# Kernel optimization log

Measured on AMD Instinct MI355X. Metric: run time of the kernel, lower is better.

The kernel has to match this reference:

```python
import jax, jax.numpy as jnp
import numpy as np

EMBED_DIM = 1024
BATCH = 4
SEQ = 4096


def setup_inputs() -> dict:
    key = jax.random.key(0)
    k1, k2, k3, k4 = jax.random.split(key, 4)
    return {
        "inputs": jax.random.normal(k1, (BATCH, SEQ, EMBED_DIM), dtype=jnp.float32),
        "Wq": jax.random.normal(k2, (EMBED_DIM, EMBED_DIM), dtype=jnp.float32),
        "Wk": jax.random.normal(k3, (EMBED_DIM, EMBED_DIM), dtype=jnp.float32),
        "Wv": jax.random.normal(k4, (EMBED_DIM, EMBED_DIM), dtype=jnp.float32),
    }


def reference(inputs, Wq, Wk, Wv):
    # inputs: [B, N, D]
    d = inputs.shape[-1]
    q = inputs @ Wq  # [B, N, D]
    k = inputs @ Wk
    v = inputs @ Wv
    scale = 1.0 / jnp.sqrt(jnp.asarray(d, dtype=inputs.dtype))
    logits = jnp.einsum("bnd,bmd->bnm", q, k) * scale  # [B, N, N]
    scores = jax.nn.softmax(logits, axis=-1)
    out = jnp.einsum("bnm,bmd->bnd", scores, v)  # [B, N, D]
    return out.mean(axis=-1)  # [B, N]
```

## Files before the change

### kernel.cpp

```cpp
#include <hip/hip_runtime.h>

#define EMBED 1024
#define BATCH 4
#define SEQ   4096
#define ROWS  (BATCH*SEQ)
#define CAP   128
#define TSCAN_SC 140.0f
#define TRES  160.0f

typedef __attribute__((ext_vector_type(8))) short bf16x8;
typedef __attribute__((ext_vector_type(4))) float f32x4;
typedef __attribute__((ext_vector_type(4))) int   i32x4;

static __device__ __forceinline__ unsigned short f2bf(float x) {
    unsigned u = __float_as_uint(x);
    u = (u + 0x7fffu + ((u >> 16) & 1u)) >> 16;
    return (unsigned short)u;
}
static __device__ __forceinline__ float bf2f(unsigned short h) {
    return __uint_as_float(((unsigned)h) << 16);
}
static __device__ __forceinline__ void split2(float x, unsigned short& hi, unsigned short& lo) {
    hi = f2bf(x);
    lo = f2bf(x - bf2f(hi));
}

static __device__ __forceinline__ void gll(const unsigned short* g, unsigned short* l) {
    __builtin_amdgcn_global_load_lds(
        (const __attribute__((address_space(1))) unsigned int*)g,
        (__attribute__((address_space(3))) unsigned int*)l, 16, 0, 0);
}
static __device__ __forceinline__ void gllb(const unsigned char* g, unsigned char* l) {
    __builtin_amdgcn_global_load_lds(
        (const __attribute__((address_space(1))) unsigned int*)g,
        (__attribute__((address_space(3))) unsigned int*)l, 16, 0, 0);
}
static __device__ __forceinline__ void stage_tile(unsigned short (*lds)[32],
                                                  const unsigned short* gbase,
                                                  int wave, int lane) {
#pragma unroll
    for (int c = 0; c < 2; c++) {
        int L = wave * 128 + c * 64 + lane;
        int r = L >> 2, s = L & 3;
        int g = (s - (r >> 1)) & 3;
        gll(gbase + (size_t)r * EMBED + g * 8, &lds[r][s * 8]);
    }
}
static __device__ __forceinline__ bf16x8 read_frag(const unsigned short (*lds)[32], int r, int kq) {
    int s = ((kq >> 3) + (r >> 1)) & 3;
    return *(const bf16x8*)&lds[r][s * 8];
}
static __device__ __forceinline__ void stage_tile8(unsigned char (*lds)[64],
                                                   const unsigned char* gbase,
                                                   int wave, int lane) {
#pragma unroll
    for (int c = 0; c < 2; c++) {
        int L = wave * 128 + c * 64 + lane;
        int r = L >> 2, s = L & 3;
        int g = (s - (r >> 1)) & 3;
        gllb(gbase + (size_t)r * EMBED + g * 16, &lds[r][s * 16]);
    }
}
static __device__ __forceinline__ i32x4 read_frag8(const unsigned char (*lds)[64], int r, int kseg) {
    int s = (kseg + (r >> 1)) & 3;
    return *(const i32x4*)&lds[r][s * 16];
}

__global__ void k_wvbar(const float* __restrict__ Wv, float* __restrict__ wvbar) {
    int r = blockIdx.x, t = threadIdx.x;
    float s = 0.f;
    for (int c = t; c < EMBED; c += 256) s += Wv[(size_t)r * EMBED + c];
    for (int d = 1; d < 64; d <<= 1) s += __shfl_xor(s, d);
    __shared__ float ws_[4];
    if ((t & 63) == 0) ws_[t >> 6] = s;
    __syncthreads();
    if (t == 0) wvbar[r] = (ws_[0] + ws_[1] + ws_[2] + ws_[3]) * (1.0f / EMBED);
}

__global__ __launch_bounds__(256) void k_xsplit_vmean(
    const float* __restrict__ X, const float* __restrict__ wvbar,
    unsigned short* __restrict__ Xhi, unsigned short* __restrict__ Xlo,
    float* __restrict__ vmean, int* __restrict__ cnt,
    signed char* __restrict__ X8, float* __restrict__ scaleX) {
    int row = blockIdx.x, t = threadIdx.x;
    float4 x4 = *(const float4*)(X + (size_t)row * EMBED + t * 4);
    float4 w4 = *(const float4*)(wvbar + t * 4);
    ushort4 h, l;
    split2(x4.x, h.x, l.x); split2(x4.y, h.y, l.y);
    split2(x4.z, h.z, l.z); split2(x4.w, h.w, l.w);
    *(ushort4*)(Xhi + (size_t)row * EMBED + t * 4) = h;
    *(ushort4*)(Xlo + (size_t)row * EMBED + t * 4) = l;
    float s = x4.x * w4.x + x4.y * w4.y + x4.z * w4.z + x4.w * w4.w;
    float am = fmaxf(fmaxf(fabsf(x4.x), fabsf(x4.y)), fmaxf(fabsf(x4.z), fabsf(x4.w)));
    for (int d = 1; d < 64; d <<= 1) {
        s += __shfl_xor(s, d);
        am = fmaxf(am, __shfl_xor(am, d));
    }
    __shared__ float ws_[4], wa_[4];
    if ((t & 63) == 0) { ws_[t >> 6] = s; wa_[t >> 6] = am; }
    __syncthreads();
    if (t == 0) { vmean[row] = ws_[0] + ws_[1] + ws_[2] + ws_[3]; cnt[row] = 0; }
    if (X8) {
        float bm = fmaxf(fmaxf(wa_[0], wa_[1]), fmaxf(wa_[2], wa_[3]));
        bm = fmaxf(bm, 1e-20f);
        float inv = 127.0f / bm;
        char4 q;
        q.x = (signed char)(int)rintf(x4.x * inv);
        q.y = (signed char)(int)rintf(x4.y * inv);
        q.z = (signed char)(int)rintf(x4.z * inv);
        q.w = (signed char)(int)rintf(x4.w * inv);
        *(char4*)(X8 + (size_t)row * EMBED + t * 4) = q;
        if (t == 0) scaleX[row] = bm * (1.0f / 127.0f);
    }
}

__global__ __launch_bounds__(256) void k_tquant(
    const unsigned short* __restrict__ Thi,
    signed char* __restrict__ T8, float* __restrict__ scaleT) {
    int row = blockIdx.x, t = threadIdx.x;
    ushort4 h = *(const ushort4*)(Thi + (size_t)row * EMBED + t * 4);
    float f0 = bf2f(h.x), f1 = bf2f(h.y), f2 = bf2f(h.z), f3 = bf2f(h.w);
    float am = fmaxf(fmaxf(fabsf(f0), fabsf(f1)), fmaxf(fabsf(f2), fabsf(f3)));
    for (int d = 1; d < 64; d <<= 1) am = fmaxf(am, __shfl_xor(am, d));
    __shared__ float wa_[4];
    if ((t & 63) == 0) wa_[t >> 6] = am;
    __syncthreads();
    float bm = fmaxf(fmaxf(fmaxf(wa_[0], wa_[1]), fmaxf(wa_[2], wa_[3])), 1e-20f);
    float inv = 127.0f / bm;
    char4 q;
    q.x = (signed char)(int)rintf(f0 * inv);
    q.y = (signed char)(int)rintf(f1 * inv);
    q.z = (signed char)(int)rintf(f2 * inv);
    q.w = (signed char)(int)rintf(f3 * inv);
    *(char4*)(T8 + (size_t)row * EMBED + t * 4) = q;
    if (t == 0) scaleT[row] = bm * (1.0f / 127.0f);
}

__global__ __launch_bounds__(256) void k_gemm3(
    const unsigned short* __restrict__ Ahi, const unsigned short* __restrict__ Alo,
    const unsigned short* __restrict__ BThi, const unsigned short* __restrict__ BTlo,
    unsigned short* __restrict__ Chi, unsigned short* __restrict__ Clo) {
    __shared__ unsigned short Ah[128][32], Al[128][32], Bh[128][32], Bl[128][32];
    int bx = blockIdx.x;
    int bm = bx >> 3, bn = bx & 7;
    int tid = threadIdx.x, wave = tid >> 6, lane = tid & 63;
    int wm = (wave >> 1) * 64, wn = (wave & 1) * 64;
    int mrow = lane & 15, kq = (lane >> 4) * 8;

    f32x4 zero = {0.f, 0.f, 0.f, 0.f};
    f32x4 acc[4][4];
    for (int a = 0; a < 4; a++) for (int b = 0; b < 4; b++) acc[a][b] = zero;

    const unsigned short* Abase_h = Ahi + (size_t)(bm * 128) * EMBED;
    const unsigned short* Abase_l = Alo + (size_t)(bm * 128) * EMBED;
    const unsigned short* Bbase_h = BThi + (size_t)(bn * 128) * EMBED;
    const unsigned short* Bbase_l = BTlo + (size_t)(bn * 128) * EMBED;

    for (int k0 = 0; k0 < EMBED; k0 += 32) {
        __syncthreads();
        stage_tile(Ah, Abase_h + k0, wave, lane);
        stage_tile(Al, Abase_l + k0, wave, lane);
        stage_tile(Bh, Bbase_h + k0, wave, lane);
        stage_tile(Bl, Bbase_l + k0, wave, lane);
        __syncthreads();
        bf16x8 ah[4], al[4], bh[4], bl[4];
#pragma unroll
        for (int t = 0; t < 4; t++) {
            ah[t] = read_frag(Ah, wm + t * 16 + mrow, kq);
            al[t] = read_frag(Al, wm + t * 16 + mrow, kq);
            bh[t] = read_frag(Bh, wn + t * 16 + mrow, kq);
            bl[t] = read_frag(Bl, wn + t * 16 + mrow, kq);
        }
#pragma unroll
        for (int mt = 0; mt < 4; mt++)
#pragma unroll
            for (int nt = 0; nt < 4; nt++) {
                acc[mt][nt] = __builtin_amdgcn_mfma_f32_16x16x32_bf16(ah[mt], bh[nt], acc[mt][nt], 0, 0, 0);
                acc[mt][nt] = __builtin_amdgcn_mfma_f32_16x16x32_bf16(ah[mt], bl[nt], acc[mt][nt], 0, 0, 0);
                acc[mt][nt] = __builtin_amdgcn_mfma_f32_16x16x32_bf16(al[mt], bh[nt], acc[mt][nt], 0, 0, 0);
            }
    }
#pragma unroll
    for (int mt = 0; mt < 4; mt++)
#pragma unroll
        for (int nt = 0; nt < 4; nt++)
#pragma unroll
            for (int i = 0; i < 4; i++) {
                int row = bm * 128 + wm + mt * 16 + (lane >> 4) * 4 + i;
                int col = bn * 128 + wn + nt * 16 + (lane & 15);
                unsigned short h, l; split2(acc[mt][nt][i], h, l);
                Chi[(size_t)row * EMBED + col] = h;
                Clo[(size_t)row * EMBED + col] = l;
            }
}

__global__ __launch_bounds__(256, 3) void k_scan(
    const signed char* __restrict__ T8, const signed char* __restrict__ X8,
    const float* __restrict__ scaleT, const float* __restrict__ scaleX,
    int* __restrict__ cnt, int2* __restrict__ cand) {
    __shared__ unsigned char ThA[128][64], KhA[128][64];
    __shared__ unsigned char ThB[128][64], KhB[128][64];
    __shared__ float rowmax_[2][2][64];
    __shared__ float sT_[128], sX_[128];
    int bid = blockIdx.x;
    int x   = bid & 7;
    int i   = bid >> 3;
    int kbi = i & 3;
    int qb  = (i >> 2) & 31;
    int b   = i >> 7;
    int kb  = x * 4 + kbi;
    int tid = threadIdx.x, wave = tid >> 6, lane = tid & 63;
    int wr = wave >> 1, wc = wave & 1;
    int wq = wr * 64, wk = wc * 64;
    int mrow = lane & 15, kseg = lane >> 4;
    size_t qrow0 = (size_t)b * SEQ + (size_t)qb * 128;
    size_t krow0 = (size_t)b * SEQ + (size_t)kb * 128;
    const unsigned char* Tk = (const unsigned char*)T8 + qrow0 * EMBED;
    const unsigned char* Xk = (const unsigned char*)X8 + krow0 * EMBED;

    if (tid < 128) sT_[tid] = scaleT[qrow0 + tid];
    else           sX_[tid - 128] = scaleX[krow0 + tid - 128];

    i32x4 zero = {0, 0, 0, 0};
    i32x4 acc[4][4];
    for (int a = 0; a < 4; a++) for (int c = 0; c < 4; c++) acc[a][c] = zero;

    for (int k0 = 0; k0 < EMBED; k0 += 128) {
        __syncthreads();
        stage_tile8(ThA, Tk + k0,      wave, lane);
        stage_tile8(KhA, Xk + k0,      wave, lane);
        stage_tile8(ThB, Tk + k0 + 64, wave, lane);
        stage_tile8(KhB, Xk + k0 + 64, wave, lane);
        __syncthreads();
        {
            i32x4 ah[4], bh[4];
#pragma unroll
            for (int t = 0; t < 4; t++) {
                ah[t] = read_frag8(ThA, wq + t * 16 + mrow, kseg);
                bh[t] = read_frag8(KhA, wk + t * 16 + mrow, kseg);
            }
#pragma unroll
            for (int mt = 0; mt < 4; mt++)
#pragma unroll
                for (int nt = 0; nt < 4; nt++)
                    acc[mt][nt] = __builtin_amdgcn_mfma_i32_16x16x64_i8(ah[mt], bh[nt], acc[mt][nt], 0, 0, 0);
        }
        {
            i32x4 ah[4], bh[4];
#pragma unroll
            for (int t = 0; t < 4; t++) {
                ah[t] = read_frag8(ThB, wq + t * 16 + mrow, kseg);
                bh[t] = read_frag8(KhB, wk + t * 16 + mrow, kseg);
            }
#pragma unroll
            for (int mt = 0; mt < 4; mt++)
#pragma unroll
                for (int nt = 0; nt < 4; nt++)
                    acc[mt][nt] = __builtin_amdgcn_mfma_i32_16x16x64_i8(ah[mt], bh[nt], acc[mt][nt], 0, 0, 0);
        }
    }

#pragma unroll
    for (int mt = 0; mt < 4; mt++)
#pragma unroll
        for (int i2 = 0; i2 < 4; i2++) {
            int lr = mt * 16 + (lane >> 4) * 4 + i2;
            float st = sT_[wq + lr] * 0.03125f;
            float v = -INFINITY;
#pragma unroll
            for (int nt = 0; nt < 4; nt++) {
                float sc = (float)acc[mt][nt][i2] * sX_[wk + nt * 16 + (lane & 15)];
                v = fmaxf(v, sc);
            }
            v *= st;
#pragma unroll
            for (int d = 1; d < 16; d <<= 1) v = fmaxf(v, __shfl_xor(v, d));
            if ((lane & 15) == 0) rowmax_[wc][wr][lr] = v;
        }
    __syncthreads();
#pragma unroll
    for (int mt = 0; mt < 4; mt++)
#pragma unroll
        for (int i2 = 0; i2 < 4; i2++) {
            int lr = mt * 16 + (lane >> 4) * 4 + i2;
            float st = sT_[wq + lr] * 0.03125f;
            float th = fmaxf(rowmax_[0][wr][lr], rowmax_[1][wr][lr]) - TSCAN_SC;
            int grow = (int)qrow0 + wq + lr;
            int lpos = lane & 15;
            unsigned mm[4];
            float sc[4];
#pragma unroll
            for (int nt = 0; nt < 4; nt++) {
                sc[nt] = (float)acc[mt][nt][i2] * sX_[wk + nt * 16 + lpos] * st;
                unsigned long long bal = __ballot(sc[nt] >= th);
                mm[nt] = (unsigned)((bal >> (lane & 48)) & 0xFFFFull);
            }
            int tot = __popc(mm[0]) + __popc(mm[1]) + __popc(mm[2]) + __popc(mm[3]);
            if (tot > 0) {
                int base = 0;
                if (lpos == 0) base = atomicAdd(&cnt[grow], tot);
                base = __shfl(base, lane & 48);
                int run = base;
                unsigned below = (1u << lpos) - 1u;
#pragma unroll
                for (int nt = 0; nt < 4; nt++) {
                    if (mm[nt] & (1u << lpos)) {
                        int slot = run + __popc(mm[nt] & below);
                        if (slot < CAP) {
                            int gcol = (int)krow0 + wk + nt * 16 + lpos;
                            cand[(size_t)grow * CAP + slot] =
                                make_int2(gcol, __float_as_int(sc[nt]));
                        }
                    }
                    run += __popc(mm[nt]);
                }
            }
        }
}

__global__ __launch_bounds__(256) void k_rescore(
    const unsigned short* __restrict__ Thi, const unsigned short* __restrict__ Tlo,
    const float* __restrict__ X, const float* __restrict__ vmean,
    const int* __restrict__ cnt, const int2* __restrict__ cand,
    float* __restrict__ out) {
    int wave = threadIdx.x >> 6, lane = threadIdx.x & 63;
    int row = blockIdx.x * 4 + wave;
    int c = cnt[row]; if (c > CAP) c = CAP;
    const int2* cl = cand + (size_t)row * CAP;

    float smax = -INFINITY;
    for (int j = lane; j < c; j += 64) smax = fmaxf(smax, __int_as_float(cl[j].y));
    for (int d = 1; d < 64; d <<= 1) smax = fmaxf(smax, __shfl_xor(smax, d));
    float th = smax - TRES;

    float q[16];
    {
        const unsigned short* qh = Thi + (size_t)row * EMBED + lane * 16;
        const unsigned short* ql = Tlo + (size_t)row * EMBED + lane * 16;
        bf16x8 h0 = *(const bf16x8*)qh, h1 = *(const bf16x8*)(qh + 8);
        bf16x8 l0 = *(const bf16x8*)ql, l1 = *(const bf16x8*)(ql + 8);
#pragma unroll
        for (int i = 0; i < 8; i++) {
            q[i]     = bf2f((unsigned short)h0[i]) + bf2f((unsigned short)l0[i]);
            q[i + 8] = bf2f((unsigned short)h1[i]) + bf2f((unsigned short)l1[i]);
        }
    }

    __shared__ int   sm_[4][CAP];
    __shared__ float sl_[4][CAP];
    __shared__ int   ns_[4];
    if (lane == 0) ns_[wave] = 0;
    for (int j = lane; j < c; j += 64) {
        int2 p = cl[j];
        if (__int_as_float(p.y) >= th) {
            int idx = atomicAdd(&ns_[wave], 1);
            sm_[wave][idx] = p.x;
        }
    }
    int ns = ns_[wave];
    for (int t = 0; t < ns; t++) {
        int m = sm_[wave][t];
        const float* xr = X + (size_t)m * EMBED + lane * 16;
        float4 a0 = *(const float4*)(xr);
        float4 a1 = *(const float4*)(xr + 4);
        float4 a2 = *(const float4*)(xr + 8);
        float4 a3 = *(const float4*)(xr + 12);
        float dp = q[0]*a0.x + q[1]*a0.y + q[2]*a0.z + q[3]*a0.w
                 + q[4]*a1.x + q[5]*a1.y + q[6]*a1.z + q[7]*a1.w
                 + q[8]*a2.x + q[9]*a2.y + q[10]*a2.z + q[11]*a2.w
                 + q[12]*a3.x + q[13]*a3.y + q[14]*a3.z + q[15]*a3.w;
        for (int d = 1; d < 64; d <<= 1) dp += __shfl_xor(dp, d);
        if (lane == 0) sl_[wave][t] = dp * 0.03125f;
    }
    if (lane == 0) {
        float lm = -INFINITY;
        for (int t = 0; t < ns; t++) lm = fmaxf(lm, sl_[wave][t]);
        float den = 0.f, num = 0.f;
        for (int t = 0; t < ns; t++) {
            float e = __expf(sl_[wave][t] - lm);
            den += e;
            num += e * vmean[sm_[wave][t]];
        }
        out[row] = num / den;
    }
}

extern "C" void kernel_launch(void* const* d_in, const int* in_sizes, int n_in,
                              void* d_out, int out_size, void* d_ws, size_t ws_size,
                              hipStream_t stream) {
    const float* X  = (const float*)d_in[0];
    const float* Wq = (const float*)d_in[1];
    const float* Wk = (const float*)d_in[2];
    const float* Wv = (const float*)d_in[3];
    float* out = (float*)d_out;

    char* p = (char*)d_ws;
    auto alloc = [&](size_t bytes) -> void* {
        void* q = (void*)p;
        p += (bytes + 255) & ~(size_t)255;
        return q;
    };
    unsigned short* Wqhi = (unsigned short*)alloc((size_t)EMBED * EMBED * 2);
    unsigned short* Wqlo = (unsigned short*)alloc((size_t)EMBED * EMBED * 2);
    unsigned short* Wkhi = (unsigned short*)alloc((size_t)EMBED * EMBED * 2);
    unsigned short* Wklo = (unsigned short*)alloc((size_t)EMBED * EMBED * 2);
    unsigned short* MThi = (unsigned short*)alloc((size_t)EMBED * EMBED * 2);
    unsigned short* MTlo = (unsigned short*)alloc((size_t)EMBED * EMBED * 2);
    unsigned short* Xhi  = (unsigned short*)alloc((size_t)ROWS * EMBED * 2);
    unsigned short* Xlo  = (unsigned short*)alloc((size_t)ROWS * EMBED * 2);
    unsigned short* Thi  = (unsigned short*)alloc((size_t)ROWS * EMBED * 2);
    unsigned short* Tlo  = (unsigned short*)alloc((size_t)ROWS * EMBED * 2);
    signed char*    T8   = (signed char*)alloc((size_t)ROWS * EMBED);
    signed char*    X8   = (signed char*)alloc((size_t)ROWS * EMBED);
    float* scaleT = (float*)alloc((size_t)ROWS * 4);
    float* scaleX = (float*)alloc((size_t)ROWS * 4);
    float* wvbar = (float*)alloc(EMBED * 4);
    float* vmean = (float*)alloc((size_t)ROWS * 4);
    int*   cnt   = (int*)alloc((size_t)ROWS * 4);
    int2*  cand  = (int2*)alloc((size_t)ROWS * CAP * 8);

    k_wvbar<<<EMBED, 256, 0, stream>>>(Wv, wvbar);
    k_xsplit_vmean<<<EMBED, 256, 0, stream>>>(Wq, wvbar, Wqhi, Wqlo, vmean, cnt, nullptr, nullptr);
    k_xsplit_vmean<<<EMBED, 256, 0, stream>>>(Wk, wvbar, Wkhi, Wklo, vmean, cnt, nullptr, nullptr);
    k_gemm3<<<64, 256, 0, stream>>>(Wkhi, Wklo, Wqhi, Wqlo, MThi, MTlo);
    k_xsplit_vmean<<<ROWS, 256, 0, stream>>>(X, wvbar, Xhi, Xlo, vmean, cnt, X8, scaleX);
    k_gemm3<<<1024, 256, 0, stream>>>(Xhi, Xlo, MThi, MTlo, Thi, Tlo);
    k_tquant<<<ROWS, 256, 0, stream>>>(Thi, T8, scaleT);
    k_scan<<<4096, 256, 0, stream>>>(T8, X8, scaleT, scaleX, cnt, cand);
    k_rescore<<<ROWS / 4, 256, 0, stream>>>(Thi, Tlo, X, vmean, cnt, cand, out);
}
```

Baseline: 464.0 us.

## Replace atomic per-row candidate list with fixed per-tile slot buckets

The scan kernel no longer does a global atomicAdd per row to append candidates into a shared list. Each (row, key-block half) gets its own fixed region of SLOT entries plus a count, written without atomics. The epilogue is also restructured: the scale is applied once into the accumulators, and the threshold is divided by the row scale so the per-element multiply is skipped in the compare. The rescore kernel then reads all 512 slots per row, which raises its read traffic. Candidates beyond 8 per region are dropped, so accuracy depends on that cap.

```diff
diff --git a/kernel.cpp b/kernel.cpp
--- a/kernel.cpp
+++ b/kernel.cpp
@@ -4,9 +4,11 @@
 #define BATCH 4
 #define SEQ   4096
 #define ROWS  (BATCH*SEQ)
-#define CAP   128
 #define TSCAN_SC 140.0f
 #define TRES  160.0f
+#define KB2   64
+#define SLOT  8
+#define RESCAP 192
 
 typedef __attribute__((ext_vector_type(8))) short bf16x8;
 typedef __attribute__((ext_vector_type(4))) float f32x4;
@@ -80,7 +82,7 @@
 __global__ __launch_bounds__(256) void k_xsplit_vmean(
     const float* __restrict__ X, const float* __restrict__ wvbar,
     unsigned short* __restrict__ Xhi, unsigned short* __restrict__ Xlo,
-    float* __restrict__ vmean, int* __restrict__ cnt,
+    float* __restrict__ vmean, int* __restrict__ cnt2,
     signed char* __restrict__ X8, float* __restrict__ scaleX) {
     int row = blockIdx.x, t = threadIdx.x;
     float4 x4 = *(const float4*)(X + (size_t)row * EMBED + t * 4);
@@ -99,7 +101,8 @@
     __shared__ float ws_[4], wa_[4];
     if ((t & 63) == 0) { ws_[t >> 6] = s; wa_[t >> 6] = am; }
     __syncthreads();
-    if (t == 0) { vmean[row] = ws_[0] + ws_[1] + ws_[2] + ws_[3]; cnt[row] = 0; }
+    if (t == 0) vmean[row] = ws_[0] + ws_[1] + ws_[2] + ws_[3];
+    if (t < KB2) cnt2[(size_t)row * KB2 + t] = 0;
     if (X8) {
         float bm = fmaxf(fmaxf(wa_[0], wa_[1]), fmaxf(wa_[2], wa_[3]));
         bm = fmaxf(bm, 1e-20f);
@@ -197,7 +200,7 @@
 __global__ __launch_bounds__(256, 3) void k_scan(
     const signed char* __restrict__ T8, const signed char* __restrict__ X8,
     const float* __restrict__ scaleT, const float* __restrict__ scaleX,
-    int* __restrict__ cnt, int2* __restrict__ cand) {
+    int* __restrict__ cnt2, int2* __restrict__ cand2) {
     __shared__ unsigned char ThA[128][64], KhA[128][64];
     __shared__ unsigned char ThB[128][64], KhB[128][64];
     __shared__ float rowmax_[2][2][64];
@@ -263,73 +266,73 @@
 #pragma unroll
     for (int mt = 0; mt < 4; mt++)
 #pragma unroll
+        for (int nt = 0; nt < 4; nt++) {
+            float sx = sX_[wk + nt * 16 + (lane & 15)];
+#pragma unroll
+            for (int i2 = 0; i2 < 4; i2++)
+                acc[mt][nt][i2] = __float_as_int((float)acc[mt][nt][i2] * sx);
+        }
+#pragma unroll
+    for (int mt = 0; mt < 4; mt++)
+#pragma unroll
+        for (int i2 = 0; i2 < 4; i2++) {
+            float v = -INFINITY;
+#pragma unroll
+            for (int nt = 0; nt < 4; nt++) v = fmaxf(v, __int_as_float(acc[mt][nt][i2]));
+#pragma unroll
+            for (int d = 1; d < 16; d <<= 1) v = fmaxf(v, __shfl_xor(v, d));
+            if ((lane & 15) == 0) rowmax_[wc][wr][mt * 16 + (lane >> 4) * 4 + i2] = v;
+        }
+    __syncthreads();
+#pragma unroll
+    for (int mt = 0; mt < 4; mt++)
+#pragma unroll
         for (int i2 = 0; i2 < 4; i2++) {
             int lr = mt * 16 + (lane >> 4) * 4 + i2;
             float st = sT_[wq + lr] * 0.03125f;
-            float v = -INFINITY;
-#pragma unroll
-            for (int nt = 0; nt < 4; nt++) {
-                float sc = (float)acc[mt][nt][i2] * sX_[wk + nt * 16 + (lane & 15)];
-                v = fmaxf(v, sc);
-            }
-            v *= st;
-#pragma unroll
-            for (int d = 1; d < 16; d <<= 1) v = fmaxf(v, __shfl_xor(v, d));
-            if ((lane & 15) == 0) rowmax_[wc][wr][lr] = v;
-        }
-    __syncthreads();
-#pragma unroll
-    for (int mt = 0; mt < 4; mt++)
-#pragma unroll
-        for (int i2 = 0; i2 < 4; i2++) {
-            int lr = mt * 16 + (lane >> 4) * 4 + i2;
-            float st = sT_[wq + lr] * 0.03125f;
-            float th = fmaxf(rowmax_[0][wr][lr], rowmax_[1][wr][lr]) - TSCAN_SC;
+            float thr = fmaxf(rowmax_[0][wr][lr], rowmax_[1][wr][lr]) - TSCAN_SC / st;
             int grow = (int)qrow0 + wq + lr;
             int lpos = lane & 15;
             unsigned mm[4];
-            float sc[4];
 #pragma unroll
             for (int nt = 0; nt < 4; nt++) {
-                sc[nt] = (float)acc[mt][nt][i2] * sX_[wk + nt * 16 + lpos] * st;
-                unsigned long long bal = __ballot(sc[nt] >= th);
+                unsigned long long bal = __ballot(__int_as_float(acc[mt][nt][i2]) >= thr);
                 mm[nt] = (unsigned)((bal >> (lane & 48)) & 0xFFFFull);
             }
-            int tot = __popc(mm[0]) + __popc(mm[1]) + __popc(mm[2]) + __popc(mm[3]);
-            if (tot > 0) {
-                int base = 0;
-                if (lpos == 0) base = atomicAdd(&cnt[grow], tot);
-                base = __shfl(base, lane & 48);
-                int run = base;
-                unsigned below = (1u << lpos) - 1u;
-#pragma unroll
-                for (int nt = 0; nt < 4; nt++) {
-                    if (mm[nt] & (1u << lpos)) {
-                        int slot = run + __popc(mm[nt] & below);
-                        if (slot < CAP) {
-                            int gcol = (int)krow0 + wk + nt * 16 + lpos;
-                            cand[(size_t)grow * CAP + slot] =
-                                make_int2(gcol, __float_as_int(sc[nt]));
-                        }
+            int reg = (int)((size_t)grow * KB2) + kb * 2 + wc;
+            int run = 0;
+            unsigned below = (1u << lpos) - 1u;
+#pragma unroll
+            for (int nt = 0; nt < 4; nt++) {
+                if (mm[nt] & (1u << lpos)) {
+                    int slot = run + __popc(mm[nt] & below);
+                    if (slot < SLOT) {
+                        int gcol = (int)krow0 + wk + nt * 16 + lpos;
+                        cand2[(size_t)reg * SLOT + slot] =
+                            make_int2(gcol, __float_as_int(__int_as_float(acc[mt][nt][i2]) * st));
                     }
-                    run += __popc(mm[nt]);
                 }
-            }
+                run += __popc(mm[nt]);
+            }
+            if (lpos == 0) cnt2[reg] = run < SLOT ? run : SLOT;
         }
 }
 
 __global__ __launch_bounds__(256) void k_rescore(
     const unsigned short* __restrict__ Thi, const unsigned short* __restrict__ Tlo,
     const float* __restrict__ X, const float* __restrict__ vmean,
-    const int* __restrict__ cnt, const int2* __restrict__ cand,
+    const int* __restrict__ cnt2, const int2* __restrict__ cand2,
     float* __restrict__ out) {
     int wave = threadIdx.x >> 6, lane = threadIdx.x & 63;
     int row = blockIdx.x * 4 + wave;
-    int c = cnt[row]; if (c > CAP) c = CAP;
-    const int2* cl = cand + (size_t)row * CAP;
+    const int*  c2 = cnt2  + (size_t)row * KB2;
+    const int2* cl = cand2 + (size_t)row * KB2 * SLOT;
 
     float smax = -INFINITY;
-    for (int j = lane; j < c; j += 64) smax = fmaxf(smax, __int_as_float(cl[j].y));
+    for (int j = lane; j < KB2 * SLOT; j += 64) {
+        int kb2 = j >> 3, s = j & (SLOT - 1);
+        if (s < c2[kb2]) smax = fmaxf(smax, __int_as_float(cl[j].y));
+    }
     for (int d = 1; d < 64; d <<= 1) smax = fmaxf(smax, __shfl_xor(smax, d));
     float th = smax - TRES;
 
@@ -346,18 +349,21 @@
         }
     }
 
-    __shared__ int   sm_[4][CAP];
-    __shared__ float sl_[4][CAP];
+    __shared__ int   sm_[4][RESCAP];
+    __shared__ float sl_[4][RESCAP];
     __shared__ int   ns_[4];
     if (lane == 0) ns_[wave] = 0;
-    for (int j = lane; j < c; j += 64) {
-        int2 p = cl[j];
-        if (__int_as_float(p.y) >= th) {
-            int idx = atomicAdd(&ns_[wave], 1);
-            sm_[wave][idx] = p.x;
-        }
-    }
-    int ns = ns_[wave];
+    for (int j = lane; j < KB2 * SLOT; j += 64) {
+        int kb2 = j >> 3, s = j & (SLOT - 1);
+        if (s < c2[kb2]) {
+            int2 p = cl[j];
+            if (__int_as_float(p.y) >= th) {
+                int idx = atomicAdd(&ns_[wave], 1);
+                if (idx < RESCAP) sm_[wave][idx] = p.x;
+            }
+        }
+    }
+    int ns = ns_[wave]; if (ns > RESCAP) ns = RESCAP;
     for (int t = 0; t < ns; t++) {
         int m = sm_[wave][t];
         const float* xr = X + (size_t)m * EMBED + lane * 16;
@@ -416,16 +422,16 @@
     float* scaleX = (float*)alloc((size_t)ROWS * 4);
     float* wvbar = (float*)alloc(EMBED * 4);
     float* vmean = (float*)alloc((size_t)ROWS * 4);
-    int*   cnt   = (int*)alloc((size_t)ROWS * 4);
-    int2*  cand  = (int2*)alloc((size_t)ROWS * CAP * 8);
+    int*   cnt2  = (int*)alloc((size_t)ROWS * KB2 * 4);
+    int2*  cand2 = (int2*)alloc((size_t)ROWS * KB2 * SLOT * 8);
 
     k_wvbar<<<EMBED, 256, 0, stream>>>(Wv, wvbar);
-    k_xsplit_vmean<<<EMBED, 256, 0, stream>>>(Wq, wvbar, Wqhi, Wqlo, vmean, cnt, nullptr, nullptr);
-    k_xsplit_vmean<<<EMBED, 256, 0, stream>>>(Wk, wvbar, Wkhi, Wklo, vmean, cnt, nullptr, nullptr);
+    k_xsplit_vmean<<<EMBED, 256, 0, stream>>>(Wq, wvbar, Wqhi, Wqlo, vmean, cnt2, nullptr, nullptr);
+    k_xsplit_vmean<<<EMBED, 256, 0, stream>>>(Wk, wvbar, Wkhi, Wklo, vmean, cnt2, nullptr, nullptr);
     k_gemm3<<<64, 256, 0, stream>>>(Wkhi, Wklo, Wqhi, Wqlo, MThi, MTlo);
-    k_xsplit_vmean<<<ROWS, 256, 0, stream>>>(X, wvbar, Xhi, Xlo, vmean, cnt, X8, scaleX);
+    k_xsplit_vmean<<<ROWS, 256, 0, stream>>>(X, wvbar, Xhi, Xlo, vmean, cnt2, X8, scaleX);
     k_gemm3<<<1024, 256, 0, stream>>>(Xhi, Xlo, MThi, MTlo, Thi, Tlo);
     k_tquant<<<ROWS, 256, 0, stream>>>(Thi, T8, scaleT);
-    k_scan<<<4096, 256, 0, stream>>>(T8, X8, scaleT, scaleX, cnt, cand);
-    k_rescore<<<ROWS / 4, 256, 0, stream>>>(Thi, Tlo, X, vmean, cnt, cand, out);
-}
+    k_scan<<<4096, 256, 0, stream>>>(T8, X8, scaleT, scaleX, cnt2, cand2);
+    k_rescore<<<ROWS / 4, 256, 0, stream>>>(Thi, Tlo, X, vmean, cnt2, cand2, out);
+}
```

New measurement: 450.3 us. 3.0% less time.
